# Performance work log

Measured on AMD Instinct MI355X. Metric: run time of the kernel, lower is better.

The kernel has to match this reference:

```python
import jax, jax.numpy as jnp
import numpy as np

N = 100000
E = 1600000
IN_FEATS = 128
H_FEATS = 128
NUM_CLASSES = 64
BN_EPS = 1e-5


def setup_inputs() -> dict:
    key = jax.random.key(0)
    ks = jax.random.split(key, 16)
    inp = {
        "in_feat": jax.random.normal(ks[0], (N, IN_FEATS), dtype=jnp.float32),
        "src": jax.random.randint(ks[1], (E,), 0, N, dtype=jnp.int64),
        "dst": jax.random.randint(ks[2], (E,), 0, N, dtype=jnp.int64),
        # GraphConv weights (glorot-ish scale) and biases
        "W0": jax.random.normal(ks[3], (IN_FEATS, H_FEATS), dtype=jnp.float32) / np.sqrt(IN_FEATS),
        "b0": jnp.zeros((H_FEATS,), dtype=jnp.float32),
        "W1": jax.random.normal(ks[4], (H_FEATS, H_FEATS), dtype=jnp.float32) / np.sqrt(H_FEATS),
        "b1": jnp.zeros((H_FEATS,), dtype=jnp.float32),
        "W2": jax.random.normal(ks[5], (H_FEATS, NUM_CLASSES), dtype=jnp.float32) / np.sqrt(H_FEATS),
        "b2": jnp.zeros((NUM_CLASSES,), dtype=jnp.float32),
        # BatchNorm affine params
        "gamma0": jnp.ones((H_FEATS,), dtype=jnp.float32),
        "beta0": jnp.zeros((H_FEATS,), dtype=jnp.float32),
        "gamma1": jnp.ones((H_FEATS,), dtype=jnp.float32),
        "beta1": jnp.zeros((H_FEATS,), dtype=jnp.float32),
    }
    return inp


def _graph_conv(src, dst, h, W, b):
    # DGL GraphConv, norm='both': D_dst^{-1/2} A (D_src^{-1/2} h W) + b
    ones = jnp.ones((src.shape[0],), dtype=h.dtype)
    deg_out = jnp.clip(jax.ops.segment_sum(ones, src, num_segments=N), 1.0)
    deg_in = jnp.clip(jax.ops.segment_sum(ones, dst, num_segments=N), 1.0)
    h = h * jax.lax.rsqrt(deg_out)[:, None]
    h = h @ W  # mult weight before aggregation (same math either way)
    agg = jax.ops.segment_sum(h[src], dst, num_segments=N)  # SpMM
    return agg * jax.lax.rsqrt(deg_in)[:, None] + b


def _batch_norm(h, gamma, beta):
    # BatchNorm1d in training mode: biased batch stats over the node axis
    mean = jnp.mean(h, axis=0)
    var = jnp.mean(jnp.square(h - mean), axis=0)
    return (h - mean) * jax.lax.rsqrt(var + BN_EPS) * gamma + beta


def reference(in_feat, src, dst, W0, b0, W1, b1, W2, b2, gamma0, beta0, gamma1, beta1):
    h = _graph_conv(src, dst, in_feat, W0, b0)
    h = jax.nn.relu(_batch_norm(h, gamma0, beta0))  # dropout p=0 -> identity
    h = _graph_conv(src, dst, h, W1, b1)
    h = jax.nn.relu(_batch_norm(h, gamma1, beta1))
    return _graph_conv(src, dst, h, W2, b2)
```

## Files before the change

### kernel.cpp

```cpp
#include <hip/hip_runtime.h>

#define NFEAT 128
#define BT 2048
#define BSH 9
#define BSZ 512

typedef __attribute__((ext_vector_type(8))) short short8v;
typedef __attribute__((ext_vector_type(4))) float float4v;

static inline size_t align_up(size_t x, size_t a) { return (x + a - 1) & ~(a - 1); }

__device__ inline unsigned short f2bf(float f) {
  unsigned u = __float_as_uint(f);
  u += 0x7FFF + ((u >> 16) & 1);
  return (unsigned short)(u >> 16);
}

__global__ __launch_bounds__(256) void k_bcount(const int* __restrict__ src,
                                                const int* __restrict__ dst,
                                                int* __restrict__ cnt, int E, int nb, int NBK) {
  __shared__ int hD[256], hS[256];
  const int t = threadIdx.x, b = blockIdx.x;
  hD[t] = 0; hS[t] = 0;
  __syncthreads();
  const int e0 = b * BT, e1 = min(E, e0 + BT);
  for (int e = e0 + t; e < e1; e += 256) {
    atomicAdd(&hD[dst[e] >> BSH], 1);
    atomicAdd(&hS[src[e] >> BSH], 1);
  }
  __syncthreads();
  if (t < NBK) {
    cnt[t * nb + b] = hD[t];
    cnt[(NBK + t) * nb + b] = hS[t];
  }
}

__global__ __launch_bounds__(512) void k_scanA(const int* __restrict__ in,
                                               int* __restrict__ out,
                                               int* __restrict__ bsum, int n) {
  __shared__ int tmp[512];
  const int t = threadIdx.x;
  const int i = blockIdx.x * 512 + t;
  int v = (i < n) ? in[i] : 0;
  tmp[t] = v;
  __syncthreads();
  for (int off = 1; off < 512; off <<= 1) {
    int y = (t >= off) ? tmp[t - off] : 0;
    __syncthreads();
    tmp[t] += y;
    __syncthreads();
  }
  int incl = tmp[t];
  if (i < n) out[i] = incl - v;
  if (t == 511) bsum[blockIdx.x] = incl;
}

__global__ __launch_bounds__(1024) void k_scanB(const int* __restrict__ bsum,
                                                int* __restrict__ bscan, int nb1) {
  __shared__ int tmp[1024];
  const int t = threadIdx.x;
  int v = (t < nb1) ? bsum[t] : 0;
  tmp[t] = v;
  __syncthreads();
  for (int off = 1; off < 1024; off <<= 1) {
    int y = (t >= off) ? tmp[t - off] : 0;
    __syncthreads();
    tmp[t] += y;
    __syncthreads();
  }
  bscan[t] = tmp[t] - v;
}

__global__ __launch_bounds__(512) void k_scanC(int* __restrict__ out,
                                               const int* __restrict__ bscan, int n) {
  const int i = blockIdx.x * 512 + threadIdx.x;
  if (i < n) out[i] += bscan[blockIdx.x];
}

__global__ __launch_bounds__(256) void k_bplace(const int* __restrict__ src,
                                                const int* __restrict__ dst,
                                                const int* __restrict__ off,
                                                int* __restrict__ buf, int E, int nb, int NBK) {
  __shared__ int cD[256], cS[256];
  const int t = threadIdx.x, b = blockIdx.x;
  if (t < NBK) {
    cD[t] = off[t * nb + b];
    cS[t] = off[(NBK + t) * nb + b];
  }
  __syncthreads();
  const int e0 = b * BT, e1 = min(E, e0 + BT);
  for (int e = e0 + t; e < e1; e += 256) {
    int s = src[e];
    int d = dst[e];
    int pD = atomicAdd(&cD[d >> BSH], 1);
    buf[pD] = ((d & (BSZ - 1)) << 17) | s;
    int pS = atomicAdd(&cS[s >> BSH], 1);
    buf[pS] = s;
  }
}

__global__ __launch_bounds__(256) void k_bcsr(const int* __restrict__ buf,
                                              const int* __restrict__ off,
                                              int* __restrict__ row_ptr,
                                              float* __restrict__ rsq_in,
                                              int* __restrict__ col,
                                              int E, int nb, int NBK, int N) {
  const int k = blockIdx.x, t = threadIdx.x;
  const int lo = off[k * nb];
  const int hi = (k + 1 < NBK) ? off[(k + 1) * nb] : E;
  __shared__ int cnt[BSZ];
  __shared__ int sc[BSZ];
  __shared__ int part[64];
  cnt[t] = 0; cnt[t + 256] = 0;
  __syncthreads();
  for (int e = lo + t; e < hi; e += 256) atomicAdd(&cnt[((unsigned)buf[e]) >> 17], 1);
  __syncthreads();
  if (t < 64) {
    int r = 0;
#pragma unroll
    for (int j = 0; j < 8; ++j) r += cnt[t * 8 + j];
    part[t] = r;
  }
  __syncthreads();
  if (t == 0) {
    int run = 0;
    for (int i = 0; i < 64; ++i) { int v = part[i]; part[i] = run; run += v; }
  }
  __syncthreads();
  if (t < 64) {
    int run = part[t];
#pragma unroll
    for (int j = 0; j < 8; ++j) { int v = cnt[t * 8 + j]; sc[t * 8 + j] = run; run += v; }
  }
  __syncthreads();
  for (int idx = t; idx < BSZ; idx += 256) {
    int n = (k << BSH) + idx;
    if (n < N) {
      row_ptr[n] = lo + sc[idx];
      int c = cnt[idx]; if (c < 1) c = 1;
      rsq_in[n] = 1.0f / sqrtf((float)c);
    }
    cnt[idx] = sc[idx];
  }
  if (k == NBK - 1 && t == 0) row_ptr[N] = E;
  __syncthreads();
  for (int e = lo + t; e < hi; e += 256) {
    int w = buf[e];
    int p = atomicAdd(&cnt[((unsigned)w) >> 17], 1);
    col[lo + p] = w & 0x1FFFF;
  }
}

__global__ __launch_bounds__(256) void k_bdeg(const int* __restrict__ buf,
                                              const int* __restrict__ off,
                                              float* __restrict__ rsq_out,
                                              int E, int nb, int NBK, int N) {
  const int k = blockIdx.x, t = threadIdx.x;
  const int lo = off[(NBK + k) * nb];
  const int hi = (k + 1 < NBK) ? off[(NBK + k + 1) * nb] : 2 * E;
  __shared__ int cnt[BSZ];
  cnt[t] = 0; cnt[t + 256] = 0;
  __syncthreads();
  for (int e = lo + t; e < hi; e += 256) atomicAdd(&cnt[buf[e] & (BSZ - 1)], 1);
  __syncthreads();
  for (int idx = t; idx < BSZ; idx += 256) {
    int n = (k << BSH) + idx;
    if (n < N) {
      int c = cnt[idx]; if (c < 1) c = 1;
      rsq_out[n] = 1.0f / sqrtf((float)c);
    }
  }
}

__global__ __launch_bounds__(256) void k_wprep(const float* __restrict__ W0,
                                               const float* __restrict__ W1,
                                               const float* __restrict__ W2,
                                               unsigned short* __restrict__ Wt0,
                                               unsigned short* __restrict__ Wt1,
                                               unsigned short* __restrict__ Wt2) {
  int t = blockIdx.x * 256 + threadIdx.x;
  if (t < 16384) {
    int c = t >> 7, k = t & 127;
    Wt0[c * 128 + k] = f2bf(W0[k * 128 + c]);
  } else if (t < 32768) {
    int u = t - 16384;
    int c = u >> 7, k = u & 127;
    Wt1[c * 128 + k] = f2bf(W1[k * 128 + c]);
  } else if (t < 40960) {
    int u = t - 32768;
    int c = u >> 7, k = u & 127;
    Wt2[c * 128 + k] = f2bf(W2[k * 64 + c]);
  }
}

template <int CC>
__global__ __launch_bounds__(256) void k_gemm_mfma(
    const float* __restrict__ X, const unsigned short* __restrict__ Wt,
    unsigned short* __restrict__ Ybf, const float* __restrict__ rsq_out,
    const float* __restrict__ bnscale, const float* __restrict__ bnshift,
    int Nrows, int mode) {
  constexpr int XBYTES = 64 * 256;
  constexpr int WBYTES = CC * 256;
  __shared__ __align__(16) char lds[XBYTES + WBYTES];
  const int tid = threadIdx.x;
  const int rowBase = blockIdx.x * 64;

  for (int u = tid; u < CC * 16; u += 256) {
    int c = u >> 4, kq = u & 15;
    uint4 v = *(const uint4*)(Wt + c * 128 + kq * 8);
    int byte = (c * 256 + kq * 16) ^ ((c & 7) << 4);
    *(uint4*)(&lds[XBYTES + byte]) = v;
  }
#pragma unroll
  for (int i = 0; i < 8; ++i) {
    int u = tid + i * 256;
    int r = u >> 5, kq = u & 31;
    int gr = rowBase + r;
    float4 v = make_float4(0.f, 0.f, 0.f, 0.f);
    if (gr < Nrows) v = *(const float4*)(X + (size_t)gr * 128 + kq * 4);
    if (mode) {
      const float4 s = *(const float4*)(bnscale + kq * 4);
      const float4 h = *(const float4*)(bnshift + kq * 4);
      v.x = fmaxf(v.x * s.x + h.x, 0.f);
      v.y = fmaxf(v.y * s.y + h.y, 0.f);
      v.z = fmaxf(v.z * s.z + h.z, 0.f);
      v.w = fmaxf(v.w * s.w + h.w, 0.f);
    }
    ushort4 o;
    o.x = f2bf(v.x); o.y = f2bf(v.y); o.z = f2bf(v.z); o.w = f2bf(v.w);
    int byte = (r * 256 + kq * 8) ^ ((r & 7) << 4);
    *(ushort4*)(&lds[byte]) = o;
  }
  __syncthreads();

  const int wv = tid >> 6;
  const int l = tid & 63;
  const int l16 = l & 15, lk = l >> 4;

  short8v a[4];
  const int arow = wv * 16 + l16;
#pragma unroll
  for (int kk = 0; kk < 4; ++kk) {
    int byte = (arow * 256 + kk * 64 + lk * 16) ^ ((arow & 7) << 4);
    a[kk] = *(const short8v*)(&lds[byte]);
  }

  float4v acc[CC / 16];
#pragma unroll
  for (int ct = 0; ct < CC / 16; ++ct) acc[ct] = (float4v){0.f, 0.f, 0.f, 0.f};

#pragma unroll
  for (int ct = 0; ct < CC / 16; ++ct) {
    const int col = ct * 16 + l16;
#pragma unroll
    for (int kk = 0; kk < 4; ++kk) {
      int byte = XBYTES + ((col * 256 + kk * 64 + lk * 16) ^ ((col & 7) << 4));
      short8v b = *(const short8v*)(&lds[byte]);
      acc[ct] = __builtin_amdgcn_mfma_f32_16x16x32_bf16(a[kk], b, acc[ct], 0, 0, 0);
    }
  }

  const int row0 = rowBase + wv * 16 + lk * 4;
  float scr[4];
#pragma unroll
  for (int r = 0; r < 4; ++r) scr[r] = (row0 + r < Nrows) ? rsq_out[row0 + r] : 0.f;
#pragma unroll
  for (int ct = 0; ct < CC / 16; ++ct) {
#pragma unroll
    for (int r = 0; r < 4; ++r) {
      int row = row0 + r;
      if (row < Nrows)
        Ybf[(size_t)row * CC + ct * 16 + l16] = f2bf(acc[ct][r] * scr[r]);
    }
  }
}

template <int F>
__global__ __launch_bounds__(256) void k_spmm_bf(const int* __restrict__ row_ptr,
                                                 const int* __restrict__ colidx,
                                                 const unsigned short* __restrict__ xW,
                                                 float* __restrict__ out,
                                                 const float* __restrict__ rsq_in,
                                                 const float* __restrict__ bias, int Nrows) {
  constexpr int L = F / 8;
  const int node = blockIdx.x * (256 / L) + threadIdx.x / L;
  const int lane = threadIdx.x % L;
  if (node >= Nrows) return;
  const int e0 = row_ptr[node];
  const int e1 = row_ptr[node + 1];
  float acc[8] = {};
  int e = e0;
  for (; e + 1 < e1; e += 2) {
    int s0 = colidx[e];
    int s1 = colidx[e + 1];
    uint4 v0 = *(const uint4*)&xW[(size_t)s0 * F + lane * 8];
    uint4 v1 = *(const uint4*)&xW[(size_t)s1 * F + lane * 8];
    acc[0] += __uint_as_float(v0.x << 16); acc[1] += __uint_as_float(v0.x & 0xFFFF0000u);
    acc[2] += __uint_as_float(v0.y << 16); acc[3] += __uint_as_float(v0.y & 0xFFFF0000u);
    acc[4] += __uint_as_float(v0.z << 16); acc[5] += __uint_as_float(v0.z & 0xFFFF0000u);
    acc[6] += __uint_as_float(v0.w << 16); acc[7] += __uint_as_float(v0.w & 0xFFFF0000u);
    acc[0] += __uint_as_float(v1.x << 16); acc[1] += __uint_as_float(v1.x & 0xFFFF0000u);
    acc[2] += __uint_as_float(v1.y << 16); acc[3] += __uint_as_float(v1.y & 0xFFFF0000u);
    acc[4] += __uint_as_float(v1.z << 16); acc[5] += __uint_as_float(v1.z & 0xFFFF0000u);
    acc[6] += __uint_as_float(v1.w << 16); acc[7] += __uint_as_float(v1.w & 0xFFFF0000u);
  }
  if (e < e1) {
    int s0 = colidx[e];
    uint4 v0 = *(const uint4*)&xW[(size_t)s0 * F + lane * 8];
    acc[0] += __uint_as_float(v0.x << 16); acc[1] += __uint_as_float(v0.x & 0xFFFF0000u);
    acc[2] += __uint_as_float(v0.y << 16); acc[3] += __uint_as_float(v0.y & 0xFFFF0000u);
    acc[4] += __uint_as_float(v0.z << 16); acc[5] += __uint_as_float(v0.z & 0xFFFF0000u);
    acc[6] += __uint_as_float(v0.w << 16); acc[7] += __uint_as_float(v0.w & 0xFFFF0000u);
  }
  const float sc = rsq_in[node];
  float4 oA, oB;
  const float4 bA = *(const float4*)&bias[lane * 8];
  const float4 bB = *(const float4*)&bias[lane * 8 + 4];
  oA.x = acc[0] * sc + bA.x; oA.y = acc[1] * sc + bA.y;
  oA.z = acc[2] * sc + bA.z; oA.w = acc[3] * sc + bA.w;
  oB.x = acc[4] * sc + bB.x; oB.y = acc[5] * sc + bB.y;
  oB.z = acc[6] * sc + bB.z; oB.w = acc[7] * sc + bB.w;
  *(float4*)&out[(size_t)node * F + lane * 8] = oA;
  *(float4*)&out[(size_t)node * F + lane * 8 + 4] = oB;
}

__global__ __launch_bounds__(256) void k_bn_stats(const float* __restrict__ h,
                                                  float* __restrict__ sum,
                                                  float* __restrict__ sumsq, int Nrows) {
  const int f = threadIdx.x & 127;
  const int half = threadIdx.x >> 7;
  float s = 0.f, ss = 0.f;
  for (int r = blockIdx.x * 2 + half; r < Nrows; r += gridDim.x * 2) {
    float v = h[(size_t)r * NFEAT + f];
    s += v;
    ss += v * v;
  }
  __shared__ float ls[256], lss[256];
  ls[threadIdx.x] = s;
  lss[threadIdx.x] = ss;
  __syncthreads();
  if (half == 0) {
    atomicAdd(&sum[f], ls[f] + ls[f + 128]);
    atomicAdd(&sumsq[f], lss[f] + lss[f + 128]);
  }
}

__global__ __launch_bounds__(128) void k_bn_final(const float* __restrict__ sum,
                                                  const float* __restrict__ sumsq,
                                                  const float* __restrict__ gamma,
                                                  const float* __restrict__ beta,
                                                  float* __restrict__ scale,
                                                  float* __restrict__ shift, int Nrows) {
  int f = threadIdx.x;
  float inv_n = 1.0f / (float)Nrows;
  float mean = sum[f] * inv_n;
  float var = sumsq[f] * inv_n - mean * mean;
  if (var < 0.f) var = 0.f;
  float sc = gamma[f] * (1.0f / sqrtf(var + 1e-5f));
  scale[f] = sc;
  shift[f] = beta[f] - mean * sc;
}

extern "C" void kernel_launch(void* const* d_in, const int* in_sizes, int n_in,
                              void* d_out, int out_size, void* d_ws, size_t ws_size,
                              hipStream_t stream) {
  const float* in_feat = (const float*)d_in[0];
  const int* src = (const int*)d_in[1];
  const int* dst = (const int*)d_in[2];
  const float* W0 = (const float*)d_in[3];
  const float* b0 = (const float*)d_in[4];
  const float* W1 = (const float*)d_in[5];
  const float* b1 = (const float*)d_in[6];
  const float* W2 = (const float*)d_in[7];
  const float* b2 = (const float*)d_in[8];
  const float* gamma0 = (const float*)d_in[9];
  const float* beta0 = (const float*)d_in[10];
  const float* gamma1 = (const float*)d_in[11];
  const float* beta1 = (const float*)d_in[12];
  float* out = (float*)d_out;

  const int N = in_sizes[0] / NFEAT;
  const int E = in_sizes[1];

  const int nb = (E + BT - 1) / BT;
  const int NBK = (N + BSZ - 1) / BSZ;
  const int L = 2 * NBK * nb;
  const int nb1 = (L + 511) / 512;

  char* p = (char*)d_ws;
  auto carve = [&](size_t bytes) {
    char* q = p;
    p += align_up(bytes, 256);
    return q;
  };
  int* cnt = (int*)carve((size_t)L * 4);
  int* off = (int*)carve((size_t)L * 4);
  int* bsum = (int*)carve(1024 * 4);
  int* bscan = (int*)carve(1024 * 4);
  int* row_ptr = (int*)carve((size_t)(N + 1) * 4);
  int* col = (int*)carve((size_t)E * 4);
  float* rsq_out = (float*)carve((size_t)N * 4);
  float* rsq_in = (float*)carve((size_t)N * 4);
  float* bn_sum0 = (float*)carve(128 * 4);
  float* bn_sumsq0 = (float*)carve(128 * 4);
  float* bn_sum1 = (float*)carve(128 * 4);
  float* bn_sumsq1 = (float*)carve(128 * 4);
  float* bn_scale0 = (float*)carve(128 * 4);
  float* bn_shift0 = (float*)carve(128 * 4);
  float* bn_scale1 = (float*)carve(128 * 4);
  float* bn_shift1 = (float*)carve(128 * 4);
  unsigned short* Wt0 = (unsigned short*)carve(16384 * 2);
  unsigned short* Wt1 = (unsigned short*)carve(16384 * 2);
  unsigned short* Wt2 = (unsigned short*)carve(8192 * 2);
  unsigned short* xWbf = (unsigned short*)carve((size_t)N * NFEAT * 2);
  float* bufB = (float*)carve((size_t)N * NFEAT * 4);
  int* buf = (int*)carve((size_t)2 * E * 4);

  hipMemsetAsync(bn_sum0, 0, 4 * 128 * 4, stream);

  k_wprep<<<160, 256, 0, stream>>>(W0, W1, W2, Wt0, Wt1, Wt2);
  k_bcount<<<nb, 256, 0, stream>>>(src, dst, cnt, E, nb, NBK);
  k_scanA<<<nb1, 512, 0, stream>>>(cnt, off, bsum, L);
  k_scanB<<<1, 1024, 0, stream>>>(bsum, bscan, nb1);
  k_scanC<<<nb1, 512, 0, stream>>>(off, bscan, L);
  k_bplace<<<nb, 256, 0, stream>>>(src, dst, off, buf, E, nb, NBK);
  k_bcsr<<<NBK, 256, 0, stream>>>(buf, off, row_ptr, rsq_in, col, E, nb, NBK, N);
  k_bdeg<<<NBK, 256, 0, stream>>>(buf, off, rsq_out, E, nb, NBK, N);

  const int GR = (N + 63) / 64;

  k_gemm_mfma<128><<<GR, 256, 0, stream>>>(in_feat, Wt0, xWbf, rsq_out,
                                           nullptr, nullptr, N, 0);
  k_spmm_bf<NFEAT><<<(N + 15) / 16, 256, 0, stream>>>(row_ptr, col, xWbf, bufB, rsq_in, b0, N);
  k_bn_stats<<<512, 256, 0, stream>>>(bufB, bn_sum0, bn_sumsq0, N);
  k_bn_final<<<1, 128, 0, stream>>>(bn_sum0, bn_sumsq0, gamma0, beta0, bn_scale0, bn_shift0, N);

  k_gemm_mfma<128><<<GR, 256, 0, stream>>>(bufB, Wt1, xWbf, rsq_out,
                                           bn_scale0, bn_shift0, N, 1);
  k_spmm_bf<NFEAT><<<(N + 15) / 16, 256, 0, stream>>>(row_ptr, col, xWbf, bufB, rsq_in, b1, N);
  k_bn_stats<<<512, 256, 0, stream>>>(bufB, bn_sum1, bn_sumsq1, N);
  k_bn_final<<<1, 128, 0, stream>>>(bn_sum1, bn_sumsq1, gamma1, beta1, bn_scale1, bn_shift1, N);

  k_gemm_mfma<64><<<GR, 256, 0, stream>>>(bufB, Wt2, xWbf, rsq_out,
                                          bn_scale1, bn_shift1, N, 1);
  k_spmm_bf<64><<<(N + 31) / 32, 256, 0, stream>>>(row_ptr, col, xWbf, out, rsq_in, b2, N);
}
```

Before: 516.5 us.

## Store hidden activations in bf16, split SpMM edges across wave lanes, deterministic BN partials

Hidden activations between layers are now stored as bf16 instead of fp32, which halves the bytes written by SpMM and read back by the BN-stats and GEMM kernels. The SpMM kernel now assigns a full 64-lane wave per node and splits that node's edges across lane groups, then reduces the groups with xor shuffles, to expose more parallel gathers. BN statistics are written as per-block partials and reduced in the final kernel instead of with atomics, which also removes the memset. The cost is extra rounding of the activations to bf16 before BatchNorm, and on low-degree nodes many lanes sit idle during the gather.

```diff
diff --git a/kernel.cpp b/kernel.cpp
--- a/kernel.cpp
+++ b/kernel.cpp
@@ -4,6 +4,7 @@
 #define BT 2048
 #define BSH 9
 #define BSZ 512
+#define NP 256
 
 typedef __attribute__((ext_vector_type(8))) short short8v;
 typedef __attribute__((ext_vector_type(4))) float float4v;
@@ -15,6 +16,11 @@
   u += 0x7FFF + ((u >> 16) & 1);
   return (unsigned short)(u >> 16);
 }
+__device__ inline unsigned pack2bf(float lo, float hi) {
+  return ((unsigned)f2bf(lo)) | (((unsigned)f2bf(hi)) << 16);
+}
+__device__ inline float bflo(unsigned u) { return __uint_as_float(u << 16); }
+__device__ inline float bfhi(unsigned u) { return __uint_as_float(u & 0xFFFF0000u); }
 
 __global__ __launch_bounds__(256) void k_bcount(const int* __restrict__ src,
                                                 const int* __restrict__ dst,
@@ -195,7 +201,8 @@
 
 template <int CC>
 __global__ __launch_bounds__(256) void k_gemm_mfma(
-    const float* __restrict__ X, const unsigned short* __restrict__ Wt,
+    const float* __restrict__ X32, const unsigned short* __restrict__ Xbf,
+    const unsigned short* __restrict__ Wt,
     unsigned short* __restrict__ Ybf, const float* __restrict__ rsq_out,
     const float* __restrict__ bnscale, const float* __restrict__ bnshift,
     int Nrows, int mode) {
@@ -211,25 +218,43 @@
     int byte = (c * 256 + kq * 16) ^ ((c & 7) << 4);
     *(uint4*)(&lds[XBYTES + byte]) = v;
   }
-#pragma unroll
-  for (int i = 0; i < 8; ++i) {
-    int u = tid + i * 256;
-    int r = u >> 5, kq = u & 31;
-    int gr = rowBase + r;
-    float4 v = make_float4(0.f, 0.f, 0.f, 0.f);
-    if (gr < Nrows) v = *(const float4*)(X + (size_t)gr * 128 + kq * 4);
-    if (mode) {
-      const float4 s = *(const float4*)(bnscale + kq * 4);
-      const float4 h = *(const float4*)(bnshift + kq * 4);
-      v.x = fmaxf(v.x * s.x + h.x, 0.f);
-      v.y = fmaxf(v.y * s.y + h.y, 0.f);
-      v.z = fmaxf(v.z * s.z + h.z, 0.f);
-      v.w = fmaxf(v.w * s.w + h.w, 0.f);
+  if (mode == 0) {
+#pragma unroll
+    for (int i = 0; i < 8; ++i) {
+      int u = tid + i * 256;
+      int r = u >> 5, kq = u & 31;
+      int gr = rowBase + r;
+      float4 v = make_float4(0.f, 0.f, 0.f, 0.f);
+      if (gr < Nrows) v = *(const float4*)(X32 + (size_t)gr * 128 + kq * 4);
+      ushort4 o;
+      o.x = f2bf(v.x); o.y = f2bf(v.y); o.z = f2bf(v.z); o.w = f2bf(v.w);
+      int byte = (r * 256 + kq * 8) ^ ((r & 7) << 4);
+      *(ushort4*)(&lds[byte]) = o;
     }
-    ushort4 o;
-    o.x = f2bf(v.x); o.y = f2bf(v.y); o.z = f2bf(v.z); o.w = f2bf(v.w);
-    int byte = (r * 256 + kq * 8) ^ ((r & 7) << 4);
-    *(ushort4*)(&lds[byte]) = o;
+  } else {
+#pragma unroll
+    for (int i = 0; i < 4; ++i) {
+      int u = tid + i * 256;
+      int r = u >> 4, kq = u & 15;
+      int gr = rowBase + r;
+      uint4 v = make_uint4(0, 0, 0, 0);
+      if (gr < Nrows) v = *(const uint4*)(Xbf + (size_t)gr * 128 + kq * 8);
+      float f0 = bflo(v.x), f1 = bfhi(v.x), f2 = bflo(v.y), f3 = bfhi(v.y);
+      float f4 = bflo(v.z), f5 = bfhi(v.z), f6 = bflo(v.w), f7 = bfhi(v.w);
+      const float4 sA = *(const float4*)(bnscale + kq * 8);
+      const float4 sB = *(const float4*)(bnscale + kq * 8 + 4);
+      const float4 hA = *(const float4*)(bnshift + kq * 8);
+      const float4 hB = *(const float4*)(bnshift + kq * 8 + 4);
+      f0 = fmaxf(f0 * sA.x + hA.x, 0.f); f1 = fmaxf(f1 * sA.y + hA.y, 0.f);
+      f2 = fmaxf(f2 * sA.z + hA.z, 0.f); f3 = fmaxf(f3 * sA.w + hA.w, 0.f);
+      f4 = fmaxf(f4 * sB.x + hB.x, 0.f); f5 = fmaxf(f5 * sB.y + hB.y, 0.f);
+      f6 = fmaxf(f6 * sB.z + hB.z, 0.f); f7 = fmaxf(f7 * sB.w + hB.w, 0.f);
+      uint4 o;
+      o.x = pack2bf(f0, f1); o.y = pack2bf(f2, f3);
+      o.z = pack2bf(f4, f5); o.w = pack2bf(f6, f7);
+      int byte = (r * 256 + kq * 16) ^ ((r & 7) << 4);
+      *(uint4*)(&lds[byte]) = o;
+    }
   }
   __syncthreads();
 
@@ -275,90 +300,125 @@
   }
 }
 
-template <int F>
-__global__ __launch_bounds__(256) void k_spmm_bf(const int* __restrict__ row_ptr,
-                                                 const int* __restrict__ colidx,
-                                                 const unsigned short* __restrict__ xW,
-                                                 float* __restrict__ out,
-                                                 const float* __restrict__ rsq_in,
-                                                 const float* __restrict__ bias, int Nrows) {
-  constexpr int L = F / 8;
-  const int node = blockIdx.x * (256 / L) + threadIdx.x / L;
-  const int lane = threadIdx.x % L;
+template <int F, int OUT_BF>
+__global__ __launch_bounds__(256) void k_spmm2(const int* __restrict__ row_ptr,
+                                               const int* __restrict__ colidx,
+                                               const unsigned short* __restrict__ xW,
+                                               void* __restrict__ outv,
+                                               const float* __restrict__ rsq_in,
+                                               const float* __restrict__ bias, int Nrows) {
+  constexpr int FL = F / 8;
+  constexpr int G = 64 / FL;
+  const int node = blockIdx.x * 4 + (threadIdx.x >> 6);
   if (node >= Nrows) return;
+  const int l = threadIdx.x & 63;
+  const int fl = l % FL, g = l / FL;
   const int e0 = row_ptr[node];
   const int e1 = row_ptr[node + 1];
   float acc[8] = {};
-  int e = e0;
-  for (; e + 1 < e1; e += 2) {
+  int e = e0 + g;
+  for (; e + G < e1; e += 2 * G) {
     int s0 = colidx[e];
-    int s1 = colidx[e + 1];
-    uint4 v0 = *(const uint4*)&xW[(size_t)s0 * F + lane * 8];
-    uint4 v1 = *(const uint4*)&xW[(size_t)s1 * F + lane * 8];
-    acc[0] += __uint_as_float(v0.x << 16); acc[1] += __uint_as_float(v0.x & 0xFFFF0000u);
-    acc[2] += __uint_as_float(v0.y << 16); acc[3] += __uint_as_float(v0.y & 0xFFFF0000u);
-    acc[4] += __uint_as_float(v0.z << 16); acc[5] += __uint_as_float(v0.z & 0xFFFF0000u);
-    acc[6] += __uint_as_float(v0.w << 16); acc[7] += __uint_as_float(v0.w & 0xFFFF0000u);
-    acc[0] += __uint_as_float(v1.x << 16); acc[1] += __uint_as_float(v1.x & 0xFFFF0000u);
-    acc[2] += __uint_as_float(v1.y << 16); acc[3] += __uint_as_float(v1.y & 0xFFFF0000u);
-    acc[4] += __uint_as_float(v1.z << 16); acc[5] += __uint_as_float(v1.z & 0xFFFF0000u);
-    acc[6] += __uint_as_float(v1.w << 16); acc[7] += __uint_as_float(v1.w & 0xFFFF0000u);
+    int s1 = colidx[e + G];
+    uint4 v0 = *(const uint4*)&xW[(size_t)s0 * F + fl * 8];
+    uint4 v1 = *(const uint4*)&xW[(size_t)s1 * F + fl * 8];
+    acc[0] += bflo(v0.x); acc[1] += bfhi(v0.x); acc[2] += bflo(v0.y); acc[3] += bfhi(v0.y);
+    acc[4] += bflo(v0.z); acc[5] += bfhi(v0.z); acc[6] += bflo(v0.w); acc[7] += bfhi(v0.w);
+    acc[0] += bflo(v1.x); acc[1] += bfhi(v1.x); acc[2] += bflo(v1.y); acc[3] += bfhi(v1.y);
+    acc[4] += bflo(v1.z); acc[5] += bfhi(v1.z); acc[6] += bflo(v1.w); acc[7] += bfhi(v1.w);
   }
   if (e < e1) {
     int s0 = colidx[e];
-    uint4 v0 = *(const uint4*)&xW[(size_t)s0 * F + lane * 8];
-    acc[0] += __uint_as_float(v0.x << 16); acc[1] += __uint_as_float(v0.x & 0xFFFF0000u);
-    acc[2] += __uint_as_float(v0.y << 16); acc[3] += __uint_as_float(v0.y & 0xFFFF0000u);
-    acc[4] += __uint_as_float(v0.z << 16); acc[5] += __uint_as_float(v0.z & 0xFFFF0000u);
-    acc[6] += __uint_as_float(v0.w << 16); acc[7] += __uint_as_float(v0.w & 0xFFFF0000u);
-  }
+    uint4 v0 = *(const uint4*)&xW[(size_t)s0 * F + fl * 8];
+    acc[0] += bflo(v0.x); acc[1] += bfhi(v0.x); acc[2] += bflo(v0.y); acc[3] += bfhi(v0.y);
+    acc[4] += bflo(v0.z); acc[5] += bfhi(v0.z); acc[6] += bflo(v0.w); acc[7] += bfhi(v0.w);
+  }
+#pragma unroll
+  for (int m = FL; m < 64; m <<= 1) {
+#pragma unroll
+    for (int j = 0; j < 8; ++j) acc[j] += __shfl_xor(acc[j], m);
+  }
+  if (g != 0) return;
   const float sc = rsq_in[node];
-  float4 oA, oB;
-  const float4 bA = *(const float4*)&bias[lane * 8];
-  const float4 bB = *(const float4*)&bias[lane * 8 + 4];
-  oA.x = acc[0] * sc + bA.x; oA.y = acc[1] * sc + bA.y;
-  oA.z = acc[2] * sc + bA.z; oA.w = acc[3] * sc + bA.w;
-  oB.x = acc[4] * sc + bB.x; oB.y = acc[5] * sc + bB.y;
-  oB.z = acc[6] * sc + bB.z; oB.w = acc[7] * sc + bB.w;
-  *(float4*)&out[(size_t)node * F + lane * 8] = oA;
-  *(float4*)&out[(size_t)node * F + lane * 8 + 4] = oB;
-}
-
-__global__ __launch_bounds__(256) void k_bn_stats(const float* __restrict__ h,
-                                                  float* __restrict__ sum,
-                                                  float* __restrict__ sumsq, int Nrows) {
-  const int f = threadIdx.x & 127;
-  const int half = threadIdx.x >> 7;
-  float s = 0.f, ss = 0.f;
-  for (int r = blockIdx.x * 2 + half; r < Nrows; r += gridDim.x * 2) {
-    float v = h[(size_t)r * NFEAT + f];
-    s += v;
-    ss += v * v;
-  }
-  __shared__ float ls[256], lss[256];
-  ls[threadIdx.x] = s;
-  lss[threadIdx.x] = ss;
-  __syncthreads();
-  if (half == 0) {
-    atomicAdd(&sum[f], ls[f] + ls[f + 128]);
-    atomicAdd(&sumsq[f], lss[f] + lss[f + 128]);
-  }
-}
-
-__global__ __launch_bounds__(128) void k_bn_final(const float* __restrict__ sum,
-                                                  const float* __restrict__ sumsq,
+  const float4 bA = *(const float4*)&bias[fl * 8];
+  const float4 bB = *(const float4*)&bias[fl * 8 + 4];
+  float o0 = acc[0] * sc + bA.x, o1 = acc[1] * sc + bA.y;
+  float o2 = acc[2] * sc + bA.z, o3 = acc[3] * sc + bA.w;
+  float o4 = acc[4] * sc + bB.x, o5 = acc[5] * sc + bB.y;
+  float o6 = acc[6] * sc + bB.z, o7 = acc[7] * sc + bB.w;
+  if (OUT_BF) {
+    uint4 w;
+    w.x = pack2bf(o0, o1); w.y = pack2bf(o2, o3);
+    w.z = pack2bf(o4, o5); w.w = pack2bf(o6, o7);
+    *(uint4*)&((unsigned short*)outv)[(size_t)node * F + fl * 8] = w;
+  } else {
+    float* out = (float*)outv;
+    *(float4*)&out[(size_t)node * F + fl * 8] = make_float4(o0, o1, o2, o3);
+    *(float4*)&out[(size_t)node * F + fl * 8 + 4] = make_float4(o4, o5, o6, o7);
+  }
+}
+
+__global__ __launch_bounds__(256) void k_bn_stats_bf(const unsigned short* __restrict__ h,
+                                                     float* __restrict__ psum,
+                                                     float* __restrict__ pssq, int Nrows) {
+  const int t = threadIdx.x;
+  const int fs = t & 15;
+  const int rg = t >> 4;
+  float s[8] = {}, ss[8] = {};
+  for (int r = blockIdx.x * 16 + rg; r < Nrows; r += gridDim.x * 16) {
+    uint4 v = *(const uint4*)&h[(size_t)r * 128 + fs * 8];
+    float f0 = bflo(v.x), f1 = bfhi(v.x), f2 = bflo(v.y), f3 = bfhi(v.y);
+    float f4 = bflo(v.z), f5 = bfhi(v.z), f6 = bflo(v.w), f7 = bfhi(v.w);
+    s[0] += f0; ss[0] += f0 * f0; s[1] += f1; ss[1] += f1 * f1;
+    s[2] += f2; ss[2] += f2 * f2; s[3] += f3; ss[3] += f3 * f3;
+    s[4] += f4; ss[4] += f4 * f4; s[5] += f5; ss[5] += f5 * f5;
+    s[6] += f6; ss[6] += f6 * f6; s[7] += f7; ss[7] += f7 * f7;
+  }
+#pragma unroll
+  for (int m = 16; m < 64; m <<= 1) {
+#pragma unroll
+    for (int j = 0; j < 8; ++j) { s[j] += __shfl_xor(s[j], m); ss[j] += __shfl_xor(ss[j], m); }
+  }
+  __shared__ float lsum[4][128], lssq[4][128];
+  const int wv = t >> 6, wl = t & 63;
+  if (wl < 16) {
+#pragma unroll
+    for (int j = 0; j < 8; ++j) { lsum[wv][wl * 8 + j] = s[j]; lssq[wv][wl * 8 + j] = ss[j]; }
+  }
+  __syncthreads();
+  if (t < 128) {
+    psum[(size_t)blockIdx.x * 128 + t] = lsum[0][t] + lsum[1][t] + lsum[2][t] + lsum[3][t];
+    pssq[(size_t)blockIdx.x * 128 + t] = lssq[0][t] + lssq[1][t] + lssq[2][t] + lssq[3][t];
+  }
+}
+
+__global__ __launch_bounds__(256) void k_bn_final(const float* __restrict__ psum,
+                                                  const float* __restrict__ pssq,
                                                   const float* __restrict__ gamma,
                                                   const float* __restrict__ beta,
                                                   float* __restrict__ scale,
                                                   float* __restrict__ shift, int Nrows) {
-  int f = threadIdx.x;
-  float inv_n = 1.0f / (float)Nrows;
-  float mean = sum[f] * inv_n;
-  float var = sumsq[f] * inv_n - mean * mean;
-  if (var < 0.f) var = 0.f;
-  float sc = gamma[f] * (1.0f / sqrtf(var + 1e-5f));
-  scale[f] = sc;
-  shift[f] = beta[f] - mean * sc;
+  const int t = threadIdx.x;
+  const int f = t & 127, half = t >> 7;
+  float s = 0.f, ss = 0.f;
+  for (int b = half * (NP / 2); b < (half + 1) * (NP / 2); ++b) {
+    s += psum[(size_t)b * 128 + f];
+    ss += pssq[(size_t)b * 128 + f];
+  }
+  __shared__ float ls[2][128], lss[2][128];
+  ls[half][f] = s; lss[half][f] = ss;
+  __syncthreads();
+  if (t < 128) {
+    float sum = ls[0][t] + ls[1][t];
+    float sumsq = lss[0][t] + lss[1][t];
+    float inv_n = 1.0f / (float)Nrows;
+    float mean = sum * inv_n;
+    float var = sumsq * inv_n - mean * mean;
+    if (var < 0.f) var = 0.f;
+    float sc = gamma[t] * (1.0f / sqrtf(var + 1e-5f));
+    scale[t] = sc;
+    shift[t] = beta[t] - mean * sc;
+  }
 }
 
 extern "C" void kernel_launch(void* const* d_in, const int* in_sizes, int n_in,
@@ -401,10 +461,10 @@
   int* col = (int*)carve((size_t)E * 4);
   float* rsq_out = (float*)carve((size_t)N * 4);
   float* rsq_in = (float*)carve((size_t)N * 4);
-  float* bn_sum0 = (float*)carve(128 * 4);
-  float* bn_sumsq0 = (float*)carve(128 * 4);
-  float* bn_sum1 = (float*)carve(128 * 4);
-  float* bn_sumsq1 = (float*)carve(128 * 4);
+  float* psum0 = (float*)carve((size_t)NP * 128 * 4);
+  float* pssq0 = (float*)carve((size_t)NP * 128 * 4);
+  float* psum1 = (float*)carve((size_t)NP * 128 * 4);
+  float* pssq1 = (float*)carve((size_t)NP * 128 * 4);
   float* bn_scale0 = (float*)carve(128 * 4);
   float* bn_shift0 = (float*)carve(128 * 4);
   float* bn_scale1 = (float*)carve(128 * 4);
@@ -413,10 +473,8 @@
   unsigned short* Wt1 = (unsigned short*)carve(16384 * 2);
   unsigned short* Wt2 = (unsigned short*)carve(8192 * 2);
   unsigned short* xWbf = (unsigned short*)carve((size_t)N * NFEAT * 2);
-  float* bufB = (float*)carve((size_t)N * NFEAT * 4);
+  unsigned short* hbf = (unsigned short*)carve((size_t)N * NFEAT * 2);
   int* buf = (int*)carve((size_t)2 * E * 4);
-
-  hipMemsetAsync(bn_sum0, 0, 4 * 128 * 4, stream);
 
   k_wprep<<<160, 256, 0, stream>>>(W0, W1, W2, Wt0, Wt1, Wt2);
   k_bcount<<<nb, 256, 0, stream>>>(src, dst, cnt, E, nb, NBK);
@@ -428,20 +486,21 @@
   k_bdeg<<<NBK, 256, 0, stream>>>(buf, off, rsq_out, E, nb, NBK, N);
 
   const int GR = (N + 63) / 64;
-
-  k_gemm_mfma<128><<<GR, 256, 0, stream>>>(in_feat, Wt0, xWbf, rsq_out,
+  const int GS = (N + 3) / 4;
+
+  k_gemm_mfma<128><<<GR, 256, 0, stream>>>(in_feat, nullptr, Wt0, xWbf, rsq_out,
                                            nullptr, nullptr, N, 0);
-  k_spmm_bf<NFEAT><<<(N + 15) / 16, 256, 0, stream>>>(row_ptr, col, xWbf, bufB, rsq_in, b0, N);
-  k_bn_stats<<<512, 256, 0, stream>>>(bufB, bn_sum0, bn_sumsq0, N);
-  k_bn_final<<<1, 128, 0, stream>>>(bn_sum0, bn_sumsq0, gamma0, beta0, bn_scale0, bn_shift0, N);
-
-  k_gemm_mfma<128><<<GR, 256, 0, stream>>>(bufB, Wt1, xWbf, rsq_out,
+  k_spmm2<128, 1><<<GS, 256, 0, stream>>>(row_ptr, col, xWbf, hbf, rsq_in, b0, N);
+  k_bn_stats_bf<<<NP, 256, 0, stream>>>(hbf, psum0, pssq0, N);
+  k_bn_final<<<1, 256, 0, stream>>>(psum0, pssq0, gamma0, beta0, bn_scale0, bn_shift0, N);
+
+  k_gemm_mfma<128><<<GR, 256, 0, stream>>>(nullptr, hbf, Wt1, xWbf, rsq_out,
                                            bn_scale0, bn_shift0, N, 1);
-  k_spmm_bf<NFEAT><<<(N + 15) / 16, 256, 0, stream>>>(row_ptr, col, xWbf, bufB, rsq_in, b1, N);
-  k_bn_stats<<<512, 256, 0, stream>>>(bufB, bn_sum1, bn_sumsq1, N);
-  k_bn_final<<<1, 128, 0, stream>>>(bn_sum1, bn_sumsq1, gamma1, beta1, bn_scale1, bn_shift1, N);
-
-  k_gemm_mfma<64><<<GR, 256, 0, stream>>>(bufB, Wt2, xWbf, rsq_out,
+  k_spmm2<128, 1><<<GS, 256, 0, stream>>>(row_ptr, col, xWbf, hbf, rsq_in, b1, N);
+  k_bn_stats_bf<<<NP, 256, 0, stream>>>(hbf, psum1, pssq1, N);
+  k_bn_final<<<1, 256, 0, stream>>>(psum1, pssq1, gamma1, beta1, bn_scale1, bn_shift1, N);
+
+  k_gemm_mfma<64><<<GR, 256, 0, stream>>>(nullptr, hbf, Wt2, xWbf, rsq_out,
                                           bn_scale1, bn_shift1, N, 1);
-  k_spmm_bf<64><<<(N + 31) / 32, 256, 0, stream>>>(row_ptr, col, xWbf, out, rsq_in, b2, N);
-}
+  k_spmm2<64, 0><<<GS, 256, 0, stream>>>(row_ptr, col, xWbf, out, rsq_in, b2, N);
+}
```

Result: no change. 517.7 us (+0.2%).
